# Performance work log

Measured on AMD Instinct MI355X. Metric: run time of the kernel, lower is better.

## Reference

```python
import jax, jax.numpy as jnp
import numpy as np

B, I, T = 8192, 128, 21
H1, H2, H3 = 256, 256, 128


def _init(key, shape, fan_in):
    # torch-style uniform(-1/sqrt(fan_in), 1/sqrt(fan_in))
    bound = 1.0 / np.sqrt(fan_in)
    return jax.random.uniform(key, shape, jnp.float32, -bound, bound)


def setup_inputs() -> dict:
    key = jax.random.key(0)
    ks = jax.random.split(key, 16)
    x = jax.random.normal(ks[0], (B, I, T), jnp.float32)
    d = {"x": x}
    # stacked LSTM weights (PyTorch layout: W_ih (4H, in), gate order i,f,g,o)
    d["W1_ih"] = _init(ks[1], (4 * H1, I), H1)
    d["b1_ih"] = _init(ks[2], (4 * H1,), H1)
    d["b1_hh"] = _init(ks[3], (4 * H1,), H1)
    d["W2_ih"] = _init(ks[4], (4 * H2, H1), H2)
    d["b2_ih"] = _init(ks[5], (4 * H2,), H2)
    d["b2_hh"] = _init(ks[6], (4 * H2,), H2)
    d["W3_ih"] = _init(ks[7], (4 * H3, H2), H3)
    d["b3_ih"] = _init(ks[8], (4 * H3,), H3)
    d["b3_hh"] = _init(ks[9], (4 * H3,), H3)
    d["fc1_w"] = _init(ks[10], (1, H3), H3)
    d["fc1_b"] = _init(ks[11], (1,), H3)
    d["fc2_w"] = _init(ks[12], (T, T), T)
    d["fc2_b"] = _init(ks[13], (T,), T)
    return d


def _lstm_cell_step(xt, W_ih, b_ih, b_hh):
    # single timestep with h0 = c0 = 0, so the W_hh @ h0 term vanishes
    gates = xt @ W_ih.T + (b_ih + b_hh)          # (B, 21, 4H)
    i, f, g, o = jnp.split(gates, 4, axis=-1)    # torch gate order i,f,g,o
    c = jax.nn.sigmoid(i) * jnp.tanh(g)          # f * c0 = 0
    return jax.nn.sigmoid(o) * jnp.tanh(c)


def reference(x, W1_ih, b1_ih, b1_hh, W2_ih, b2_ih, b2_hh,
              W3_ih, b3_ih, b3_hh, fc1_w, fc1_b, fc2_w, fc2_b):
    # fold the 21 independent single-step columns into the batch dim
    xt = jnp.transpose(x, (0, 2, 1))             # (B, 21, I)
    h1 = _lstm_cell_step(xt, W1_ih, b1_ih, b1_hh)   # (B, 21, H1)
    h2 = _lstm_cell_step(h1, W2_ih, b2_ih, b2_hh)   # (B, 21, H2)
    h3 = _lstm_cell_step(h2, W3_ih, b3_ih, b3_hh)   # (B, 21, H3)
    y = h3 @ fc1_w.T + fc1_b                     # (B, 21, 1)
    y = y[..., 0][:, None, :]                    # (B, 1, 21)  == x_torch
    out = y @ fc2_w.T + fc2_b                    # (B, 1, 21)
    return out
```

## Files before the change

kernel.cpp:

```cpp
#include <hip/hip_runtime.h>
#include <hip/hip_bf16.h>
#include <stdint.h>


typedef __attribute__((ext_vector_type(8))) short bf16x8;
typedef __attribute__((ext_vector_type(4))) float f32x4;

#define M_ROWS 172032
#define BATCH  8192

__device__ __forceinline__ float bf2f(unsigned short u) {
    union { unsigned int i; float f; } v; v.i = ((unsigned int)u) << 16; return v.f;
}
__device__ __forceinline__ unsigned short f2bf(float f) {
    union { float f; unsigned int i; } v; v.f = f;
    unsigned int r = v.i + 0x7fffu + ((v.i >> 16) & 1u);
    return (unsigned short)(r >> 16);
}
__device__ __forceinline__ float sigmoidf_(float x) {
    return __builtin_amdgcn_rcpf(1.0f + __expf(-x));
}
__device__ __forceinline__ float tanhf_(float x) {
    x = fminf(fmaxf(x, -20.0f), 20.0f);
    float e = __expf(-2.0f * x);
    return (1.0f - e) * __builtin_amdgcn_rcpf(1.0f + e);
}

__global__ __launch_bounds__(256) void k_convert(
    const float* __restrict__ src, unsigned short* __restrict__ dst, int n4)
{
    int i = blockIdx.x * 256 + threadIdx.x;
    if (i < n4) {
        float4 v = ((const float4*)src)[i];
        ushort4 o;
        o.x = f2bf(v.x); o.y = f2bf(v.y); o.z = f2bf(v.z); o.w = f2bf(v.w);
        ((ushort4*)dst)[i] = o;
    }
}

__global__ __launch_bounds__(256) void k_transpose(
    const float* __restrict__ x, unsigned short* __restrict__ xt)
{
    __shared__ unsigned short tile[128 * 22];
    const int b = blockIdx.x, tid = threadIdx.x;
    const float* xb = x + (size_t)b * 2688;
    for (int idx = tid; idx < 2688; idx += 256) {
        int i = idx / 21, t = idx - i * 21;
        tile[i * 22 + t] = f2bf(xb[idx]);
    }
    __syncthreads();
    unsigned short* xtb = xt + (size_t)b * 2688;
    for (int idx = tid; idx < 2688; idx += 256) {
        int t = idx >> 7, i = idx & 127;
        xtb[t * 128 + i] = tile[i * 22 + t];
    }
}

template<int K, int HG>
__global__ __launch_bounds__(256, 2) void k_gemm_act(
    const unsigned short* __restrict__ A,
    const unsigned short* __restrict__ W,
    const float* __restrict__ bih,
    const float* __restrict__ bhh,
    unsigned short* __restrict__ Hout)
{
    __shared__ __align__(16) unsigned short As[128 * 64];
    __shared__ __align__(16) unsigned short Ws[192 * 64];
    __shared__ float Bs[192];

    const int tid  = threadIdx.x;
    const int wave = tid >> 6;
    const int lane = tid & 63;
    const int wm = wave >> 1;
    const int wn = wave & 1;
    const int r0 = blockIdx.x * 128;
    const int c0 = blockIdx.y * 64;

    if (tid < 192) {
        int g = tid >> 6, c = tid & 63;
        int gbase = (g == 0) ? 0 : (g + 1) * HG;
        int idx = gbase + c0 + c;
        Bs[tid] = bih[idx] + bhh[idx];
    }

    f32x4 acc[3][4][2];
#pragma unroll
    for (int g = 0; g < 3; ++g)
#pragma unroll
        for (int m = 0; m < 4; ++m)
#pragma unroll
            for (int n = 0; n < 2; ++n)
                acc[g][m][n] = (f32x4){0.f, 0.f, 0.f, 0.f};

#pragma unroll
    for (int kk = 0; kk < K; kk += 64) {
        bf16x8 av[4], wv[6];
#pragma unroll
        for (int i = 0; i < 4; ++i) {
            int q = tid + 256 * i;
            int row = q >> 3, off = (q & 7) * 8;
            av[i] = *(const bf16x8*)(A + (size_t)(r0 + row) * K + kk + off);
        }
#pragma unroll
        for (int i = 0; i < 6; ++i) {
            int q = tid + 256 * i;
            int lrow = q >> 3, off = (q & 7) * 8;
            int gate = lrow >> 6, n = lrow & 63;
            int gbase = (gate == 0) ? 0 : (gate + 1) * HG;
            wv[i] = *(const bf16x8*)(W + (size_t)(gbase + c0 + n) * K + kk + off);
        }
        if (kk) __syncthreads();
#pragma unroll
        for (int i = 0; i < 4; ++i) { int q = tid + 256 * i; *(bf16x8*)&As[q * 8] = av[i]; }
#pragma unroll
        for (int i = 0; i < 6; ++i) { int q = tid + 256 * i; *(bf16x8*)&Ws[q * 8] = wv[i]; }
        __syncthreads();

#pragma unroll
        for (int ks = 0; ks < 64; ks += 32) {
            bf16x8 af[4];
            bf16x8 bfr[3][2];
            const int koff = ks + (lane >> 4) * 8;
            const int rsel = lane & 15;
#pragma unroll
            for (int m = 0; m < 4; ++m)
                af[m] = *(const bf16x8*)&As[(wm * 64 + m * 16 + rsel) * 64 + koff];
#pragma unroll
            for (int g = 0; g < 3; ++g)
#pragma unroll
                for (int n = 0; n < 2; ++n)
                    bfr[g][n] = *(const bf16x8*)&Ws[(g * 64 + wn * 32 + n * 16 + rsel) * 64 + koff];
#pragma unroll
            for (int g = 0; g < 3; ++g)
#pragma unroll
                for (int m = 0; m < 4; ++m)
#pragma unroll
                    for (int n = 0; n < 2; ++n)
                        acc[g][m][n] = __builtin_amdgcn_mfma_f32_16x16x32_bf16(
                            af[m], bfr[g][n], acc[g][m][n], 0, 0, 0);
        }
    }

    const int quad = lane >> 4;
    const int csel = lane & 15;
#pragma unroll
    for (int m = 0; m < 4; ++m) {
#pragma unroll
        for (int n = 0; n < 2; ++n) {
            int cloc = wn * 32 + n * 16 + csel;
            float bi = Bs[cloc], bg = Bs[64 + cloc], bo = Bs[128 + cloc];
            f32x4 vi = acc[0][m][n], vg = acc[1][m][n], vo = acc[2][m][n];
#pragma unroll
            for (int r = 0; r < 4; ++r) {
                int row = r0 + wm * 64 + m * 16 + quad * 4 + r;
                float cv = sigmoidf_(vi[r] + bi) * tanhf_(vg[r] + bg);
                float h  = sigmoidf_(vo[r] + bo) * tanhf_(cv);
                Hout[(size_t)row * HG + c0 + cloc] = f2bf(h);
            }
        }
    }
}

#define FSTR 169
__global__ __launch_bounds__(256) void k_final(
    const unsigned short* __restrict__ h3,
    const float* __restrict__ fc1w,
    const float* __restrict__ fc1b,
    const float* __restrict__ fc2w,
    const float* __restrict__ fc2b,
    float* __restrict__ out)
{
    __shared__ unsigned short ht[128 * FSTR];
    __shared__ float fwl[128];
    __shared__ float yl[168];
    __shared__ float f2l[441];
    __shared__ float f2bl[21];

    const int tid = threadIdx.x;
    const int b0 = blockIdx.x * 8;

    if (tid < 128) fwl[tid] = fc1w[tid];
    for (int i = tid; i < 441; i += 256) f2l[i] = fc2w[i];
    if (tid < 21) f2bl[tid] = fc2b[tid];

    const unsigned int* hsrc = (const unsigned int*)(h3 + (size_t)b0 * 2688);
    for (int gi = tid; gi < 10752; gi += 256) {
        unsigned int v = hsrc[gi];
        int e = gi * 2;
        int task = e >> 7;
        int c = e & 127;
        ht[c * FSTR + task] = (unsigned short)(v & 0xffffu);
        ht[(c + 1) * FSTR + task] = (unsigned short)(v >> 16);
    }
    __syncthreads();

    const float f1b = fc1b[0];
    if (tid < 168) {
        float s = f1b;
#pragma unroll 8
        for (int c = 0; c < 128; ++c)
            s += fwl[c] * bf2f(ht[c * FSTR + tid]);
        yl[tid] = s;
    }
    __syncthreads();
    if (tid < 168) {
        int bloc = tid / 21;
        int tp = tid - bloc * 21;
        float s = f2bl[tp];
#pragma unroll
        for (int t = 0; t < 21; ++t)
            s += yl[bloc * 21 + t] * f2l[tp * 21 + t];
        out[(size_t)(b0 + bloc) * 21 + tp] = s;
    }
}

extern "C" void kernel_launch(void* const* d_in, const int* in_sizes, int n_in,
                              void* d_out, int out_size, void* d_ws, size_t ws_size,
                              hipStream_t stream)
{
    const float* x    = (const float*)d_in[0];
    const float* W1   = (const float*)d_in[1];
    const float* b1i  = (const float*)d_in[2];
    const float* b1h  = (const float*)d_in[3];
    const float* W2   = (const float*)d_in[4];
    const float* b2i  = (const float*)d_in[5];
    const float* b2h  = (const float*)d_in[6];
    const float* W3   = (const float*)d_in[7];
    const float* b3i  = (const float*)d_in[8];
    const float* b3h  = (const float*)d_in[9];
    const float* fc1w = (const float*)d_in[10];
    const float* fc1b = (const float*)d_in[11];
    const float* fc2w = (const float*)d_in[12];
    const float* fc2b = (const float*)d_in[13];
    float* out = (float*)d_out;

    unsigned short* Wc1 = (unsigned short*)d_ws;
    unsigned short* Wc2 = Wc1 + 131072;
    unsigned short* Wc3 = Wc2 + 262144;
    unsigned short* buf = Wc3 + 131072;

    int C = 1;
    while (C < 64 && 1048576 + (size_t)(M_ROWS / C) * 1536 > ws_size) C <<= 1;
    const int R  = M_ROWS / C;
    const int Bc = BATCH / C;

    unsigned short* xt = buf;
    unsigned short* h1 = xt + (size_t)R * 128;
    unsigned short* h2 = h1 + (size_t)R * 256;
    unsigned short* h3 = h2 + (size_t)R * 256;

    k_convert<<<128, 256, 0, stream>>>(W1, Wc1, 32768);
    k_convert<<<256, 256, 0, stream>>>(W2, Wc2, 65536);
    k_convert<<<128, 256, 0, stream>>>(W3, Wc3, 32768);

    for (int c = 0; c < C; ++c) {
        const float* xc = x + (size_t)c * Bc * 2688;
        k_transpose<<<Bc, 256, 0, stream>>>(xc, xt);
        k_gemm_act<128, 256><<<dim3(R / 128, 4), 256, 0, stream>>>(xt, Wc1, b1i, b1h, h1);
        k_gemm_act<256, 256><<<dim3(R / 128, 4), 256, 0, stream>>>(h1, Wc2, b2i, b2h, h2);
        k_gemm_act<256, 128><<<dim3(R / 128, 2), 256, 0, stream>>>(h2, Wc3, b3i, b3h, h3);
        k_final<<<Bc / 8, 256, 0, stream>>>(h3, fc1w, fc1b, fc2w, fc2b,
                                            out + (size_t)c * Bc * 21);
    }
}
```

Measured before the change: 430.9 us.

## Load GEMM tiles directly into LDS and swap grid order for A reuse

Global-to-register-to-LDS staging in the fused LSTM gate GEMM is replaced with direct global_load_lds 16-byte transfers, so tile data no longer passes through VGPRs. The grid is also transposed so column blocks vary fastest and blocks that share the same A row tile run close together, which should improve L2 reuse of activations. The direct loads are issued only after the previous iteration's barrier, so global-load latency no longer overlaps with the previous compute. Register pressure drops, which may allow higher occupancy.

```diff
diff --git a/kernel.cpp b/kernel.cpp
--- a/kernel.cpp
+++ b/kernel.cpp
@@ -24,6 +24,11 @@
     x = fminf(fmaxf(x, -20.0f), 20.0f);
     float e = __expf(-2.0f * x);
     return (1.0f - e) * __builtin_amdgcn_rcpf(1.0f + e);
+}
+__device__ __forceinline__ void g2l16(const unsigned short* g, unsigned short* l) {
+    __builtin_amdgcn_global_load_lds(
+        (const __attribute__((address_space(1))) unsigned int*)g,
+        (__attribute__((address_space(3))) unsigned int*)l, 16, 0, 0);
 }
 
 __global__ __launch_bounds__(256) void k_convert(
@@ -73,8 +78,8 @@
     const int lane = tid & 63;
     const int wm = wave >> 1;
     const int wn = wave & 1;
-    const int r0 = blockIdx.x * 128;
-    const int c0 = blockIdx.y * 64;
+    const int c0 = blockIdx.x * 64;
+    const int r0 = blockIdx.y * 128;
 
     if (tid < 192) {
         int g = tid >> 6, c = tid & 63;
@@ -92,28 +97,26 @@
             for (int n = 0; n < 2; ++n)
                 acc[g][m][n] = (f32x4){0.f, 0.f, 0.f, 0.f};
 
+    const int l_hi = lane >> 3;
+    const int l_lo = (lane & 7) * 8;
+
 #pragma unroll
     for (int kk = 0; kk < K; kk += 64) {
-        bf16x8 av[4], wv[6];
+        if (kk) __syncthreads();
 #pragma unroll
         for (int i = 0; i < 4; ++i) {
-            int q = tid + 256 * i;
-            int row = q >> 3, off = (q & 7) * 8;
-            av[i] = *(const bf16x8*)(A + (size_t)(r0 + row) * K + kk + off);
+            int row = wave * 32 + i * 8;
+            g2l16(A + (size_t)(r0 + row + l_hi) * K + kk + l_lo, &As[row * 64]);
         }
 #pragma unroll
         for (int i = 0; i < 6; ++i) {
-            int q = tid + 256 * i;
-            int lrow = q >> 3, off = (q & 7) * 8;
-            int gate = lrow >> 6, n = lrow & 63;
+            int row  = wave * 48 + i * 8;
+            int lrow = row + l_hi;
+            int gate = lrow >> 6;
+            int n    = lrow & 63;
             int gbase = (gate == 0) ? 0 : (gate + 1) * HG;
-            wv[i] = *(const bf16x8*)(W + (size_t)(gbase + c0 + n) * K + kk + off);
-        }
-        if (kk) __syncthreads();
-#pragma unroll
-        for (int i = 0; i < 4; ++i) { int q = tid + 256 * i; *(bf16x8*)&As[q * 8] = av[i]; }
-#pragma unroll
-        for (int i = 0; i < 6; ++i) { int q = tid + 256 * i; *(bf16x8*)&Ws[q * 8] = wv[i]; }
+            g2l16(W + (size_t)(gbase + c0 + n) * K + kk + l_lo, &Ws[row * 64]);
+        }
         __syncthreads();
 
 #pragma unroll
@@ -256,9 +259,9 @@
     for (int c = 0; c < C; ++c) {
         const float* xc = x + (size_t)c * Bc * 2688;
         k_transpose<<<Bc, 256, 0, stream>>>(xc, xt);
-        k_gemm_act<128, 256><<<dim3(R / 128, 4), 256, 0, stream>>>(xt, Wc1, b1i, b1h, h1);
-        k_gemm_act<256, 256><<<dim3(R / 128, 4), 256, 0, stream>>>(h1, Wc2, b2i, b2h, h2);
-        k_gemm_act<256, 128><<<dim3(R / 128, 2), 256, 0, stream>>>(h2, Wc3, b3i, b3h, h3);
+        k_gemm_act<128, 256><<<dim3(4, R / 128), 256, 0, stream>>>(xt, Wc1, b1i, b1h, h1);
+        k_gemm_act<256, 256><<<dim3(4, R / 128), 256, 0, stream>>>(h1, Wc2, b2i, b2h, h2);
+        k_gemm_act<256, 128><<<dim3(2, R / 128), 256, 0, stream>>>(h2, Wc3, b3i, b3h, h3);
         k_final<<<Bc / 8, 256, 0, stream>>>(h3, fc1w, fc1b, fc2w, fc2b,
                                             out + (size_t)c * Bc * 21);
     }
```

Result: slower. 442.1 us (+2.6%).
